# Performance work log

Measured on AMD Instinct MI355X. Metric: run time of the kernel, lower is better.

The kernel has to match this reference:

```python
import jax, jax.numpy as jnp
import numpy as np

T = 4            # number of node types (len(output_sizes))
N = 16384        # nodes per type
D_IN = 512       # input_size
D_H = 1024       # hidden_size
OUT_SIZES = (128, 96, 64, 32)
MAX_OUT = max(OUT_SIZES)


def setup_inputs() -> dict:
    key = jax.random.key(0)
    ks = jax.random.split(key, 16)
    inp = {}
    for t in range(T):
        inp[f"x{t}"] = jax.random.normal(ks[t], (N, D_IN), jnp.float32)
    # nodes are grouped by type (sorted), matching the padded dict layout
    inp["node_type"] = jnp.repeat(jnp.arange(T, dtype=jnp.int64), N)
    # layer1: per-type Linear(input_size, hidden_size) (apply_net)
    inp["W1"] = jax.random.normal(ks[4], (T, D_IN, D_H), jnp.float32) * 0.02
    inp["b1"] = jnp.zeros((T, D_H), jnp.float32)
    # layer2: per-type Linear(hidden_size, out_size_t)
    for t in range(T):
        inp[f"W2_{t}"] = jax.random.normal(ks[5 + t], (D_H, OUT_SIZES[t]), jnp.float32) * 0.02
        inp[f"b2_{t}"] = jnp.zeros((OUT_SIZES[t],), jnp.float32)
    return inp


def reference(x0, x1, x2, x3, node_type, W1, b1,
              W2_0, b2_0, W2_1, b2_1, W2_2, b2_2, W2_3, b2_3):
    # Per-type gather is implicit: x{t} already holds the features of the
    # nodes whose node_type == t (node_type is sorted/blocked).
    xs = jnp.stack([x0, x1, x2, x3])                       # [T, N, D_IN]
    # apply_net: layer1 per type + activation (batched grouped-GEMM)
    h = jax.nn.relu(jnp.einsum('tni,tih->tnh', xs, W1) + b1[:, None, :])  # [T, N, D_H]
    W2s = (W2_0, W2_1, W2_2, W2_3)
    b2s = (b2_0, b2_1, b2_2, b2_3)
    outs = []
    for t in range(T):  # fixed small set of structurally distinct heads
        o = h[t] @ W2s[t] + b2s[t]                         # [N, out_t]
        outs.append(jnp.pad(o, ((0, 0), (0, MAX_OUT - o.shape[1]))))  # _pad to MAX_OUT
    return jnp.stack(outs)                                 # [T, N, MAX_OUT]
```

## Files before the change

kernel.cpp:

```cpp
#include <hip/hip_runtime.h>
#include <hip/hip_bf16.h>


typedef __attribute__((ext_vector_type(8))) short short8;
typedef __attribute__((ext_vector_type(4))) float f32x4;

#define NT 4
#define NNODE 16384
#define DIN 512
#define DH 1024
#define MAXO 128

static __device__ __forceinline__ ushort f2bf(float f) {
    __hip_bfloat16 h = __float2bfloat16(f);
    return *reinterpret_cast<ushort*>(&h);
}

static __device__ __forceinline__ short8 pack8(const float4 a, const float4 b) {
    union { short8 v; ushort u[8]; } r;
    r.u[0] = f2bf(a.x); r.u[1] = f2bf(a.y); r.u[2] = f2bf(a.z); r.u[3] = f2bf(a.w);
    r.u[4] = f2bf(b.x); r.u[5] = f2bf(b.y); r.u[6] = f2bf(b.z); r.u[7] = f2bf(b.w);
    return r.v;
}

#define GLD(gsrc, ldst)                                                        \
    __builtin_amdgcn_global_load_lds(                                          \
        (const __attribute__((address_space(1))) void*)(gsrc),                 \
        (__attribute__((address_space(3))) void*)(ldst), 16, 0, 0)

__global__ __launch_bounds__(256) void cvt_w_t_kernel(
    const float* __restrict__ in, ushort* __restrict__ out,
    int R, int Cin, size_t in_tstride, size_t out_tstride) {
    __shared__ float tile[32][33];
    const int t = blockIdx.z;
    in += (size_t)t * in_tstride;
    out += (size_t)t * out_tstride;
    const int c0 = blockIdx.x * 32, r0 = blockIdx.y * 32;
    const int cx = threadIdx.x & 31;
    const int ry = threadIdx.x >> 5;
#pragma unroll
    for (int j = 0; j < 4; ++j) {
        int rr = ry + j * 8;
        int c = c0 + cx;
        tile[rr][cx] = (c < Cin) ? in[(size_t)(r0 + rr) * Cin + c] : 0.0f;
    }
    __syncthreads();
#pragma unroll
    for (int j = 0; j < 4; ++j) {
        int cc = ry + j * 8;
        out[(size_t)(c0 + cc) * R + r0 + cx] = f2bf(tile[cx][cc]);
    }
}

__global__ void pad_b2_kernel(const float* __restrict__ b0, const float* __restrict__ b1,
                              const float* __restrict__ b2, const float* __restrict__ b3,
                              float* __restrict__ out) {
    const int i = threadIdx.x;
    const int t = i >> 7, n = i & 127;
    const int sz[4] = {128, 96, 64, 32};
    const float* b = (t == 0) ? b0 : (t == 1) ? b1 : (t == 2) ? b2 : b3;
    out[i] = (n < sz[t]) ? b[n] : 0.0f;
}

template <int BN, bool AFP32, bool RELU, bool OUTBF16>
__global__ __launch_bounds__(512, 1) void gemmf(
    const void* __restrict__ A0, const void* __restrict__ A1,
    const void* __restrict__ A2, const void* __restrict__ A3,
    const ushort* __restrict__ Bbase, const float* __restrict__ biasbase,
    void* __restrict__ Cbase, int N, int K, int MT,
    size_t strideA, size_t strideB, size_t strideBias, size_t strideC) {
    constexpr int NF = BN / 64;
    constexpr int NBC = BN * 8 / 512;
    constexpr int ABYTES = 256 * 64 * 2;
    constexpr int BBYTES = BN * 64 * 2;
    constexpr int BUF = ABYTES + BBYTES;
    __shared__ char lds[2 * BUF];

    const int cpx = gridDim.x >> 3;
    const int g = blockIdx.x;
    const int wg = (g & 7) * cpx + (g >> 3);
    const int NTL = N / BN;
    const int t = wg / (MT * NTL);
    const int rmn = wg % (MT * NTL);
    const int m0 = (rmn / NTL) * 256;
    const int n0 = (rmn % NTL) * BN;

    const float* Af = (const float*)((t == 0) ? A0 : (t == 1) ? A1
                                   : (t == 2) ? A2 : A3);
    const ushort* Ab = (const ushort*)A0 + (size_t)t * strideA;
    const ushort* Bp = Bbase + (size_t)t * strideB;
    const float* bias = biasbase + (size_t)t * strideBias;

    const int tid = threadIdx.x;
    const int lane = tid & 63;
    const int w = tid >> 6;
    const int wm = w >> 2, wn = w & 3;
    const int lrow = lane & 15, lgrp = lane >> 4;

    const float* af32src[4];
    const ushort* abfsrc[4];
    int adst[4];
#pragma unroll
    for (int j = 0; j < 4; ++j) {
        const int c = j * 512 + tid;
        const int r = c >> 3;
        const int c8 = c & 7;
        const int cb = (c8 * 16) ^ ((r & 7) << 4);
        if (AFP32) {
            af32src[j] = Af + (size_t)(m0 + r) * K + c8 * 8;
            adst[j] = r * 128 + cb;
        } else {
            abfsrc[j] = Ab + (size_t)(m0 + r) * K + (cb >> 1);
            adst[j] = c * 16;
        }
    }
    const ushort* bsrc[NBC];
    int bdst[NBC];
#pragma unroll
    for (int j = 0; j < NBC; ++j) {
        const int c = j * 512 + tid;
        const int r = c >> 3;
        const int cb = ((c & 7) * 16) ^ ((r & 7) << 4);
        bsrc[j] = Bp + (size_t)(n0 + r) * K + (cb >> 1);
        bdst[j] = ABYTES + c * 16;
    }

    f32x4 acc[8][NF] = {};
    const int NK = K / 64;
    float4 fa[4][2];

    if (AFP32) {
#pragma unroll
        for (int j = 0; j < 4; ++j) {
            fa[j][0] = *reinterpret_cast<const float4*>(af32src[j]);
            fa[j][1] = *reinterpret_cast<const float4*>(af32src[j] + 4);
        }
#pragma unroll
        for (int j = 0; j < NBC; ++j) GLD(bsrc[j], lds + bdst[j]);
#pragma unroll
        for (int j = 0; j < 4; ++j)
            *reinterpret_cast<short8*>(lds + adst[j]) = pack8(fa[j][0], fa[j][1]);
    } else {
#pragma unroll
        for (int j = 0; j < 4; ++j) GLD(abfsrc[j], lds + adst[j]);
#pragma unroll
        for (int j = 0; j < NBC; ++j) GLD(bsrc[j], lds + bdst[j]);
    }
    asm volatile("s_waitcnt vmcnt(0) lgkmcnt(0)" ::: "memory");
    __builtin_amdgcn_s_barrier();
    asm volatile("" ::: "memory");

    for (int i = 0; i < NK; ++i) {
        const char* cu_ = lds + (i & 1) * BUF;
        char* nx_ = lds + ((i + 1) & 1) * BUF;
        const int ktn = (i + 1) * 64;
        const bool st = (i + 1 < NK);

        if (st) {
            if (AFP32) {
#pragma unroll
                for (int j = 0; j < 4; ++j) {
                    fa[j][0] = *reinterpret_cast<const float4*>(af32src[j] + ktn);
                    fa[j][1] = *reinterpret_cast<const float4*>(af32src[j] + ktn + 4);
                }
            } else {
#pragma unroll
                for (int j = 0; j < 4; ++j) GLD(abfsrc[j] + ktn, nx_ + adst[j]);
            }
#pragma unroll
            for (int j = 0; j < NBC; ++j) GLD(bsrc[j] + ktn, nx_ + bdst[j]);
        }

#pragma unroll
        for (int kkk = 0; kkk < 2; ++kkk) {
            short8 bfr[NF], af[8];
#pragma unroll
            for (int ni = 0; ni < NF; ++ni) {
                const int br = wn * (NF * 16) + ni * 16 + lrow;
                const int kb = (kkk * 64 + lgrp * 16) ^ ((br & 7) << 4);
                bfr[ni] = *(const short8*)(cu_ + ABYTES + br * 128 + kb);
            }
#pragma unroll
            for (int ml = 0; ml < 8; ++ml) {
                const int ar = wm * 128 + ml * 16 + lrow;
                const int kb = (kkk * 64 + lgrp * 16) ^ ((ar & 7) << 4);
                af[ml] = *(const short8*)(cu_ + ar * 128 + kb);
            }
#pragma unroll
            for (int ml = 0; ml < 8; ++ml)
#pragma unroll
                for (int ni = 0; ni < NF; ++ni)
                    acc[ml][ni] = __builtin_amdgcn_mfma_f32_16x16x32_bf16(
                        bfr[ni], af[ml], acc[ml][ni], 0, 0, 0);
        }

        if (st) {
            if (AFP32) {
#pragma unroll
                for (int j = 0; j < 4; ++j)
                    *reinterpret_cast<short8*>(nx_ + adst[j]) =
                        pack8(fa[j][0], fa[j][1]);
            }
            asm volatile("s_waitcnt vmcnt(0) lgkmcnt(0)" ::: "memory");
            __builtin_amdgcn_s_barrier();
            asm volatile("" ::: "memory");
        }
    }

    const int wnoff = n0 + wn * (NF * 16);
    const int wmoff = m0 + wm * 128;
#pragma unroll
    for (int ni = 0; ni < NF; ++ni) {
        const int ncol = wnoff + ni * 16 + lgrp * 4;
        const float4 bv = *reinterpret_cast<const float4*>(&bias[ncol]);
#pragma unroll
        for (int mi = 0; mi < 8; ++mi) {
            const int row = wmoff + mi * 16 + lrow;
            float v0 = acc[mi][ni][0] + bv.x;
            float v1 = acc[mi][ni][1] + bv.y;
            float v2 = acc[mi][ni][2] + bv.z;
            float v3 = acc[mi][ni][3] + bv.w;
            if (RELU) {
                v0 = fmaxf(v0, 0.0f); v1 = fmaxf(v1, 0.0f);
                v2 = fmaxf(v2, 0.0f); v3 = fmaxf(v3, 0.0f);
            }
            const size_t base = (size_t)t * strideC + (size_t)row * N + ncol;
            if (OUTBF16) {
                uint2 p;
                p.x = (uint)f2bf(v0) | ((uint)f2bf(v1) << 16);
                p.y = (uint)f2bf(v2) | ((uint)f2bf(v3) << 16);
                *reinterpret_cast<uint2*>(&((ushort*)Cbase)[base]) = p;
            } else {
                float4 p = {v0, v1, v2, v3};
                *reinterpret_cast<float4*>(&((float*)Cbase)[base]) = p;
            }
        }
    }
}

extern "C" void kernel_launch(void* const* d_in, const int* in_sizes, int n_in,
                              void* d_out, int out_size, void* d_ws, size_t ws_size,
                              hipStream_t stream) {
    const float* x0 = (const float*)d_in[0];
    const float* x1 = (const float*)d_in[1];
    const float* x2 = (const float*)d_in[2];
    const float* x3 = (const float*)d_in[3];
    const float* W1 = (const float*)d_in[5];
    const float* b1 = (const float*)d_in[6];
    const float* W2[4] = {(const float*)d_in[7], (const float*)d_in[9],
                          (const float*)d_in[11], (const float*)d_in[13]};
    const float* b2[4] = {(const float*)d_in[8], (const float*)d_in[10],
                          (const float*)d_in[12], (const float*)d_in[14]};

    char* ws = (char*)d_ws;
    ushort* H   = (ushort*)ws;
    ushort* W1T = (ushort*)(ws + 134217728ull);
    ushort* W2T = (ushort*)(ws + 134217728ull + 4194304ull);
    float*  b2p = (float*)(ws + 134217728ull + 4194304ull + 1048576ull);

    cvt_w_t_kernel<<<dim3(32, 16, 4), 256, 0, stream>>>(
        W1, W1T, DIN, DH, (size_t)DIN * DH, (size_t)DH * DIN);
    const int osz[4] = {128, 96, 64, 32};
    for (int t = 0; t < 4; ++t)
        cvt_w_t_kernel<<<dim3(4, 32, 1), 256, 0, stream>>>(
            W2[t], W2T + (size_t)t * MAXO * DH, DH, osz[t], 0, 0);
    pad_b2_kernel<<<1, 512, 0, stream>>>(b2[0], b2[1], b2[2], b2[3], b2p);

    gemmf<256, true, true, true><<<1024, 512, 0, stream>>>(
        x0, x1, x2, x3, W1T, b1, H,
        DH, DIN, NNODE / 256,
        0, (size_t)DH * DIN, (size_t)DH, (size_t)NNODE * DH);

    gemmf<128, false, false, false><<<256, 512, 0, stream>>>(
        H, H, H, H, W2T, b2p, d_out,
        MAXO, DH, NNODE / 256,
        (size_t)NNODE * DH, (size_t)MAXO * DH, (size_t)MAXO,
        (size_t)NNODE * MAXO);
}
```

Baseline: 175.9 us.

## Prefetch fp32 A tile two stages ahead and merge W2/bias prep kernels

Result: faster. 153.7 us (median of 2 runs) (-12.6%).

```diff
diff --git a/kernel.cpp b/kernel.cpp
--- a/kernel.cpp
+++ b/kernel.cpp
@@ -52,14 +52,37 @@
     }
 }
 
-__global__ void pad_b2_kernel(const float* __restrict__ b0, const float* __restrict__ b1,
-                              const float* __restrict__ b2, const float* __restrict__ b3,
-                              float* __restrict__ out) {
-    const int i = threadIdx.x;
-    const int t = i >> 7, n = i & 127;
-    const int sz[4] = {128, 96, 64, 32};
-    const float* b = (t == 0) ? b0 : (t == 1) ? b1 : (t == 2) ? b2 : b3;
-    out[i] = (n < sz[t]) ? b[n] : 0.0f;
+__global__ __launch_bounds__(256) void cvt_w2_kernel(
+    const float* __restrict__ w0, const float* __restrict__ w1,
+    const float* __restrict__ w2, const float* __restrict__ w3,
+    const float* __restrict__ c0_, const float* __restrict__ c1_,
+    const float* __restrict__ c2_, const float* __restrict__ c3_,
+    ushort* __restrict__ out, float* __restrict__ b2p) {
+    __shared__ float tile[32][33];
+    const int t = blockIdx.z;
+    const int Cin = (t == 0) ? 128 : (t == 1) ? 96 : (t == 2) ? 64 : 32;
+    const float* in = (t == 0) ? w0 : (t == 1) ? w1 : (t == 2) ? w2 : w3;
+    ushort* o = out + (size_t)t * MAXO * DH;
+    const int c0 = blockIdx.x * 32, r0 = blockIdx.y * 32;
+    const int cx = threadIdx.x & 31;
+    const int ry = threadIdx.x >> 5;
+#pragma unroll
+    for (int j = 0; j < 4; ++j) {
+        int rr = ry + j * 8;
+        int c = c0 + cx;
+        tile[rr][cx] = (c < Cin) ? in[(size_t)(r0 + rr) * Cin + c] : 0.0f;
+    }
+    __syncthreads();
+#pragma unroll
+    for (int j = 0; j < 4; ++j) {
+        int cc = ry + j * 8;
+        o[(size_t)(c0 + cc) * DH + r0 + cx] = f2bf(tile[cx][cc]);
+    }
+    if (blockIdx.x == 0 && blockIdx.y == 0 && threadIdx.x < 128) {
+        const float* b = (t == 0) ? c0_ : (t == 1) ? c1_ : (t == 2) ? c2_ : c3_;
+        const int n = threadIdx.x;
+        b2p[t * 128 + n] = (n < Cin) ? b[n] : 0.0f;
+    }
 }
 
 template <int BN, bool AFP32, bool RELU, bool OUTBF16>
@@ -75,6 +98,7 @@
     constexpr int BBYTES = BN * 64 * 2;
     constexpr int BUF = ABYTES + BBYTES;
     __shared__ char lds[2 * BUF];
+    static_assert(!AFP32 || NBC == 4, "AFP32 path assumes BN=256");
 
     const int cpx = gridDim.x >> 3;
     const int g = blockIdx.x;
@@ -137,16 +161,26 @@
         }
 #pragma unroll
         for (int j = 0; j < NBC; ++j) GLD(bsrc[j], lds + bdst[j]);
+        asm volatile("s_waitcnt vmcnt(4)" ::: "memory");
 #pragma unroll
         for (int j = 0; j < 4; ++j)
             *reinterpret_cast<short8*>(lds + adst[j]) = pack8(fa[j][0], fa[j][1]);
+        asm volatile("" ::: "memory");
+        if (NK > 1) {
+#pragma unroll
+            for (int j = 0; j < 4; ++j) {
+                fa[j][0] = *reinterpret_cast<const float4*>(af32src[j] + 64);
+                fa[j][1] = *reinterpret_cast<const float4*>(af32src[j] + 68);
+            }
+        }
+        asm volatile("s_waitcnt vmcnt(8) lgkmcnt(0)" ::: "memory");
     } else {
 #pragma unroll
         for (int j = 0; j < 4; ++j) GLD(abfsrc[j], lds + adst[j]);
 #pragma unroll
         for (int j = 0; j < NBC; ++j) GLD(bsrc[j], lds + bdst[j]);
-    }
-    asm volatile("s_waitcnt vmcnt(0) lgkmcnt(0)" ::: "memory");
+        asm volatile("s_waitcnt vmcnt(0) lgkmcnt(0)" ::: "memory");
+    }
     __builtin_amdgcn_s_barrier();
     asm volatile("" ::: "memory");
 
@@ -155,20 +189,30 @@
         char* nx_ = lds + ((i + 1) & 1) * BUF;
         const int ktn = (i + 1) * 64;
         const bool st = (i + 1 < NK);
+        const bool st2 = (i + 2 < NK);
 
         if (st) {
+#pragma unroll
+            for (int j = 0; j < NBC; ++j) GLD(bsrc[j] + ktn, nx_ + bdst[j]);
             if (AFP32) {
 #pragma unroll
-                for (int j = 0; j < 4; ++j) {
-                    fa[j][0] = *reinterpret_cast<const float4*>(af32src[j] + ktn);
-                    fa[j][1] = *reinterpret_cast<const float4*>(af32src[j] + ktn + 4);
+                for (int j = 0; j < 4; ++j)
+                    *reinterpret_cast<short8*>(nx_ + adst[j]) =
+                        pack8(fa[j][0], fa[j][1]);
+                asm volatile("" ::: "memory");
+                if (st2) {
+#pragma unroll
+                    for (int j = 0; j < 4; ++j) {
+                        fa[j][0] = *reinterpret_cast<const float4*>(
+                            af32src[j] + ktn + 64);
+                        fa[j][1] = *reinterpret_cast<const float4*>(
+                            af32src[j] + ktn + 68);
+                    }
                 }
             } else {
 #pragma unroll
                 for (int j = 0; j < 4; ++j) GLD(abfsrc[j] + ktn, nx_ + adst[j]);
             }
-#pragma unroll
-            for (int j = 0; j < NBC; ++j) GLD(bsrc[j] + ktn, nx_ + bdst[j]);
         }
 
 #pragma unroll
@@ -195,13 +239,10 @@
         }
 
         if (st) {
-            if (AFP32) {
-#pragma unroll
-                for (int j = 0; j < 4; ++j)
-                    *reinterpret_cast<short8*>(nx_ + adst[j]) =
-                        pack8(fa[j][0], fa[j][1]);
-            }
-            asm volatile("s_waitcnt vmcnt(0) lgkmcnt(0)" ::: "memory");
+            if (AFP32 && st2)
+                asm volatile("s_waitcnt vmcnt(8) lgkmcnt(0)" ::: "memory");
+            else
+                asm volatile("s_waitcnt vmcnt(0) lgkmcnt(0)" ::: "memory");
             __builtin_amdgcn_s_barrier();
             asm volatile("" ::: "memory");
         }
@@ -260,11 +301,8 @@
 
     cvt_w_t_kernel<<<dim3(32, 16, 4), 256, 0, stream>>>(
         W1, W1T, DIN, DH, (size_t)DIN * DH, (size_t)DH * DIN);
-    const int osz[4] = {128, 96, 64, 32};
-    for (int t = 0; t < 4; ++t)
-        cvt_w_t_kernel<<<dim3(4, 32, 1), 256, 0, stream>>>(
-            W2[t], W2T + (size_t)t * MAXO * DH, DH, osz[t], 0, 0);
-    pad_b2_kernel<<<1, 512, 0, stream>>>(b2[0], b2[1], b2[2], b2[3], b2p);
+    cvt_w2_kernel<<<dim3(4, 32, 4), 256, 0, stream>>>(
+        W2[0], W2[1], W2[2], W2[3], b2[0], b2[1], b2[2], b2[3], W2T, b2p);
 
     gemmf<256, true, true, true><<<1024, 512, 0, stream>>>(
         x0, x1, x2, x3, W1T, b1, H,
```
